# Kernel optimization log

Measured on AMD Instinct MI355X. Metric: run time of the kernel, lower is better.

Reference implementation:

```python
import jax, jax.numpy as jnp
import numpy as np

SEQ = 4096
BLOCK = 64            # sparse_block_size
BLOCKS = SEQ // BLOCK # 64 block rows/cols
NUM_ORACLES = 32
ORACLE = SEQ // NUM_ORACLES      # 128
LOCAL_BLOCKS = ORACLE // BLOCK   # 2 (sliding-window width in blocks)
PATTERN_ID = 0


def _build_block_mask(pattern_id=PATTERN_ID):
    # Mirrors DKernelPredefinedSparseAttention.__init__ create_mask((i,))
    q_pos = np.arange(BLOCKS)[:, None]
    k_pos = np.arange(BLOCKS)[None, :]
    causal = q_pos >= k_pos
    sliding = (q_pos - k_pos) < LOCAL_BLOCKS
    vert = np.zeros(BLOCKS, dtype=bool)
    real_col = int(pattern_id * ORACLE + 0.5)
    cs = real_col // BLOCK
    ce = (real_col + ORACLE) // BLOCK
    vert[cs:ce] = True
    vert[0:1] = True  # global block 0 always visible
    return causal & (sliding | vert[None, :])


def setup_inputs() -> dict:
    key = jax.random.key(0)
    kq, kk, kv = jax.random.split(key, 3)
    shape = (1, SEQ, 8, 128)  # bshd, matches module's own smoke test layout
    q = jax.random.normal(kq, shape, dtype=jnp.float32)
    k = jax.random.normal(kk, shape, dtype=jnp.float32)
    v = jax.random.normal(kv, shape, dtype=jnp.float32)
    block_mask = jnp.asarray(_build_block_mask())  # [BLOCKS, BLOCKS] bool
    return {"q": q, "k": k, "v": v, "block_mask": block_mask}


def reference(q, k, v, block_mask):
    # Expand block-level mask to token level: [S, S]
    tok_mask = jnp.repeat(jnp.repeat(block_mask, BLOCK, axis=0), BLOCK, axis=1)
    scale = 1.0 / jnp.sqrt(jnp.asarray(q.shape[-1], q.dtype))
    # bshd x bshd -> bhqk scores
    scores = jnp.einsum("bqhd,bkhd->bhqk", q, k) * scale
    neg = jnp.asarray(-1e30, scores.dtype)
    scores = jnp.where(tok_mask[None, None, :, :], scores, neg)
    probs = jax.nn.softmax(scores, axis=-1)
    out = jnp.einsum("bhqk,bkhd->bqhd", probs, v)
    return out
```

## Files before the change

### kernel.cpp

```cpp
#include <hip/hip_runtime.h>
#include <hip/hip_bf16.h>

typedef __bf16 bf16x8 __attribute__((ext_vector_type(8)));
typedef float floatx4 __attribute__((ext_vector_type(4)));

constexpr int SEQ = 4096;
constexpr int NH  = 8;
constexpr int DH  = 128;
constexpr int BLK = 64;
constexpr int QBLOCKS = SEQ / BLK;
constexpr int RS = NH * DH;
constexpr float SCALE = 0.088388347648318447f;

__device__ __forceinline__ bf16x8 load8f(const float* p) {
    float4 a = *(const float4*)p;
    float4 b = *(const float4*)(p + 4);
    bf16x8 r = { (__bf16)a.x, (__bf16)a.y, (__bf16)a.z, (__bf16)a.w,
                 (__bf16)b.x, (__bf16)b.y, (__bf16)b.z, (__bf16)b.w };
    return r;
}

__device__ __forceinline__ void stage_v(const float* __restrict__ V,
                                        int kb, int h, int n_t, int kh,
                                        __bf16* __restrict__ dst) {
    const float* base = V + (size_t)(kb * BLK + kh * 32) * RS + h * DH + n_t;
    const int nt = n_t >> 4;
    const int lbase = n_t & 15;
#pragma unroll
    for (int g = 0; g < 4; ++g) {
        bf16x8 pk;
#pragma unroll
        for (int j = 0; j < 8; ++j)
            pk[j] = (__bf16)base[(size_t)(g * 8 + j) * RS];
        __bf16* d = dst + ((size_t)((kh * 8 + nt) * 64 + lbase + 16 * g)) * 8;
        *(bf16x8*)d = pk;
    }
}

__global__ __launch_bounds__(256) void sparse_attn_kernel(
    const float* __restrict__ Q,
    const float* __restrict__ K,
    const float* __restrict__ V,
    float* __restrict__ Out)
{
    const int qb   = blockIdx.x;
    const int h    = blockIdx.y;
    const int tid  = threadIdx.x;
    const int wave = tid >> 6;
    const int lane = tid & 63;
    const int quad = lane >> 4;
    const int l16  = lane & 15;

    __shared__ __align__(16) __bf16 v_lds[2][2][8][64][8];
    __shared__ __align__(16) __bf16 p_lds[4][16][BLK + 8];

    const int n_t = tid & 127;
    const int kh  = tid >> 7;

    const int qrow = qb * BLK + wave * 16 + l16;
    const float* qp = Q + (size_t)qrow * RS + h * DH;
    bf16x8 qfrag[4];
#pragma unroll
    for (int s = 0; s < 4; ++s)
        qfrag[s] = load8f(qp + s * 32 + quad * 8);

    floatx4 o_acc[8];
#pragma unroll
    for (int n = 0; n < 8; ++n) o_acc[n] = floatx4{0.f, 0.f, 0.f, 0.f};
    float m_run[4], l_run[4];
#pragma unroll
    for (int r = 0; r < 4; ++r) { m_run[r] = -1e30f; l_run[r] = 0.f; }

    int blist[4];
    int nb = 0;
    {
        int cand[4] = {0, 1, qb - 1, qb};
        for (int i = 0; i < 4; ++i) {
            int b = cand[i];
            if (b < 0 || b > qb) continue;
            bool dup = false;
            for (int j = 0; j < nb; ++j) dup = dup || (blist[j] == b);
            if (!dup) blist[nb++] = b;
        }
    }

    stage_v(V, blist[0], h, n_t, kh, &v_lds[0][0][0][0][0]);

    for (int bi = 0; bi < nb; ++bi) {
        __syncthreads();
        if (bi + 1 < nb)
            stage_v(V, blist[bi + 1], h, n_t, kh,
                    &v_lds[(bi + 1) & 1][0][0][0][0]);

        const int kb  = blist[bi];
        const int buf = bi & 1;

        floatx4 sfrag[4];
#pragma unroll
        for (int n = 0; n < 4; ++n) {
            floatx4 c = floatx4{0.f, 0.f, 0.f, 0.f};
            const float* kp =
                K + (size_t)(kb * BLK + n * 16 + l16) * RS + h * DH;
#pragma unroll
            for (int s = 0; s < 4; ++s) {
                bf16x8 kf = load8f(kp + s * 32 + quad * 8);
                c = __builtin_amdgcn_mfma_f32_16x16x32_bf16(qfrag[s], kf, c, 0, 0, 0);
            }
            sfrag[n] = c;
        }

        float mnew[4];
#pragma unroll
        for (int r = 0; r < 4; ++r) {
            float mx = m_run[r];
#pragma unroll
            for (int n = 0; n < 4; ++n) {
                sfrag[n][r] *= SCALE;
                mx = fmaxf(mx, sfrag[n][r]);
            }
#pragma unroll
            for (int off = 1; off < 16; off <<= 1)
                mx = fmaxf(mx, __shfl_xor(mx, off, 64));
            mnew[r] = mx;
        }
#pragma unroll
        for (int r = 0; r < 4; ++r) {
            float alpha = __expf(m_run[r] - mnew[r]);
            float rs = 0.f;
#pragma unroll
            for (int n = 0; n < 4; ++n) {
                float p = __expf(sfrag[n][r] - mnew[r]);
                sfrag[n][r] = p;
                rs += p;
            }
#pragma unroll
            for (int off = 1; off < 16; off <<= 1)
                rs += __shfl_xor(rs, off, 64);
            l_run[r] = l_run[r] * alpha + rs;
            m_run[r] = mnew[r];
#pragma unroll
            for (int n = 0; n < 8; ++n) o_acc[n][r] *= alpha;
        }

#pragma unroll
        for (int n = 0; n < 4; ++n)
#pragma unroll
            for (int r = 0; r < 4; ++r)
                p_lds[wave][quad * 4 + r][n * 16 + l16] = (__bf16)sfrag[n][r];

#pragma unroll
        for (int s2 = 0; s2 < 2; ++s2) {
            bf16x8 pa = *(const bf16x8*)&p_lds[wave][l16][s2 * 32 + quad * 8];
#pragma unroll
            for (int n = 0; n < 8; ++n) {
                bf16x8 vb = *(const bf16x8*)&v_lds[buf][s2][n][lane][0];
                o_acc[n] = __builtin_amdgcn_mfma_f32_16x16x32_bf16(pa, vb, o_acc[n], 0, 0, 0);
            }
        }
    }

    const int orow_base = qb * BLK + wave * 16 + quad * 4;
#pragma unroll
    for (int r = 0; r < 4; ++r) {
        float inv = 1.f / l_run[r];
        float* op = Out + (size_t)(orow_base + r) * RS + h * DH + l16;
#pragma unroll
        for (int n = 0; n < 8; ++n)
            op[n * 16] = o_acc[n][r] * inv;
    }
}

extern "C" void kernel_launch(void* const* d_in, const int* in_sizes, int n_in,
                              void* d_out, int out_size, void* d_ws, size_t ws_size,
                              hipStream_t stream) {
    const float* Q = (const float*)d_in[0];
    const float* K = (const float*)d_in[1];
    const float* V = (const float*)d_in[2];
    float* Out = (float*)d_out;

    dim3 grid(QBLOCKS, NH);
    dim3 block(256);
    sparse_attn_kernel<<<grid, block, 0, stream>>>(Q, K, V, Out);
}
```

Before: 127.7 us.

## Split key blocks across two wave groups with split-K softmax merge

Doubles the workgroup to 512 threads, with two groups of four waves each handling alternate key blocks for the same query strip. All V blocks are staged into LDS up front instead of double-buffered. Partial softmax states are merged through LDS at the end. The P tile in LDS now uses an XOR swizzle to cut bank conflicts. This raises parallelism and shortens the serial per-block chain, at the cost of extra LDS, a merge step and duplicated Q loads.

```diff
diff --git a/kernel.cpp b/kernel.cpp
--- a/kernel.cpp
+++ b/kernel.cpp
@@ -37,39 +37,24 @@
     }
 }
 
-__global__ __launch_bounds__(256) void sparse_attn_kernel(
+__global__ __launch_bounds__(512, 4) void sparse_attn_kernel(
     const float* __restrict__ Q,
     const float* __restrict__ K,
     const float* __restrict__ V,
     float* __restrict__ Out)
 {
-    const int qb   = blockIdx.x;
-    const int h    = blockIdx.y;
-    const int tid  = threadIdx.x;
-    const int wave = tid >> 6;
-    const int lane = tid & 63;
-    const int quad = lane >> 4;
-    const int l16  = lane & 15;
-
-    __shared__ __align__(16) __bf16 v_lds[2][2][8][64][8];
-    __shared__ __align__(16) __bf16 p_lds[4][16][BLK + 8];
-
-    const int n_t = tid & 127;
-    const int kh  = tid >> 7;
-
-    const int qrow = qb * BLK + wave * 16 + l16;
-    const float* qp = Q + (size_t)qrow * RS + h * DH;
-    bf16x8 qfrag[4];
-#pragma unroll
-    for (int s = 0; s < 4; ++s)
-        qfrag[s] = load8f(qp + s * 32 + quad * 8);
-
-    floatx4 o_acc[8];
-#pragma unroll
-    for (int n = 0; n < 8; ++n) o_acc[n] = floatx4{0.f, 0.f, 0.f, 0.f};
-    float m_run[4], l_run[4];
-#pragma unroll
-    for (int r = 0; r < 4; ++r) { m_run[r] = -1e30f; l_run[r] = 0.f; }
+    const int qb    = blockIdx.x;
+    const int h     = blockIdx.y;
+    const int tid   = threadIdx.x;
+    const int wave  = tid >> 6;
+    const int lane  = tid & 63;
+    const int strip = wave & 3;
+    const int grp   = wave >> 2;
+    const int quad  = lane >> 4;
+    const int l16   = lane & 15;
+
+    __shared__ __align__(16) __bf16 v_lds[4][2][8][64][8];
+    __shared__ __align__(16) __bf16 p_lds[8][16][64];
 
     int blist[4];
     int nb = 0;
@@ -84,89 +69,150 @@
         }
     }
 
-    stage_v(V, blist[0], h, n_t, kh, &v_lds[0][0][0][0][0]);
-
-    for (int bi = 0; bi < nb; ++bi) {
-        __syncthreads();
-        if (bi + 1 < nb)
-            stage_v(V, blist[bi + 1], h, n_t, kh,
-                    &v_lds[(bi + 1) & 1][0][0][0][0]);
-
-        const int kb  = blist[bi];
-        const int buf = bi & 1;
-
-        floatx4 sfrag[4];
-#pragma unroll
-        for (int n = 0; n < 4; ++n) {
-            floatx4 c = floatx4{0.f, 0.f, 0.f, 0.f};
-            const float* kp =
-                K + (size_t)(kb * BLK + n * 16 + l16) * RS + h * DH;
-#pragma unroll
-            for (int s = 0; s < 4; ++s) {
-                bf16x8 kf = load8f(kp + s * 32 + quad * 8);
-                c = __builtin_amdgcn_mfma_f32_16x16x32_bf16(qfrag[s], kf, c, 0, 0, 0);
-            }
-            sfrag[n] = c;
-        }
-
-        float mnew[4];
+    {
+        const int t256 = tid & 255;
+        const int n_t  = t256 & 127;
+        const int kh   = t256 >> 7;
+        const int half = tid >> 8;
+        if (half < nb)
+            stage_v(V, blist[half], h, n_t, kh, &v_lds[half][0][0][0][0]);
+        if (half + 2 < nb)
+            stage_v(V, blist[half + 2], h, n_t, kh, &v_lds[half + 2][0][0][0][0]);
+    }
+
+    const int qrow = qb * BLK + strip * 16 + l16;
+    const float* qp = Q + (size_t)qrow * RS + h * DH;
+    bf16x8 qfrag[4];
+#pragma unroll
+    for (int s = 0; s < 4; ++s)
+        qfrag[s] = load8f(qp + s * 32 + quad * 8);
+
+    floatx4 o_acc[8];
+#pragma unroll
+    for (int n = 0; n < 8; ++n) o_acc[n] = floatx4{0.f, 0.f, 0.f, 0.f};
+    float m_run[4], l_run[4];
+#pragma unroll
+    for (int r = 0; r < 4; ++r) { m_run[r] = -1e30f; l_run[r] = 0.f; }
+
+    __syncthreads();
+
+#pragma unroll
+    for (int it = 0; it < 2; ++it) {
+        const int bi = grp + 2 * it;
+        if (bi < nb) {
+            const int kb = blist[bi];
+
+            floatx4 sfrag[4];
+#pragma unroll
+            for (int n = 0; n < 4; ++n) {
+                floatx4 c = floatx4{0.f, 0.f, 0.f, 0.f};
+                const float* kp =
+                    K + (size_t)(kb * BLK + n * 16 + l16) * RS + h * DH;
+#pragma unroll
+                for (int s = 0; s < 4; ++s) {
+                    bf16x8 kf = load8f(kp + s * 32 + quad * 8);
+                    c = __builtin_amdgcn_mfma_f32_16x16x32_bf16(qfrag[s], kf, c, 0, 0, 0);
+                }
+                sfrag[n] = c;
+            }
+
+            float mnew[4];
+#pragma unroll
+            for (int r = 0; r < 4; ++r) {
+                float mx = m_run[r];
+#pragma unroll
+                for (int n = 0; n < 4; ++n) {
+                    sfrag[n][r] *= SCALE;
+                    mx = fmaxf(mx, sfrag[n][r]);
+                }
+#pragma unroll
+                for (int off = 1; off < 16; off <<= 1)
+                    mx = fmaxf(mx, __shfl_xor(mx, off, 64));
+                mnew[r] = mx;
+            }
+#pragma unroll
+            for (int r = 0; r < 4; ++r) {
+                float alpha = __expf(m_run[r] - mnew[r]);
+                float rs = 0.f;
+#pragma unroll
+                for (int n = 0; n < 4; ++n) {
+                    float p = __expf(sfrag[n][r] - mnew[r]);
+                    sfrag[n][r] = p;
+                    rs += p;
+                }
+#pragma unroll
+                for (int off = 1; off < 16; off <<= 1)
+                    rs += __shfl_xor(rs, off, 64);
+                l_run[r] = l_run[r] * alpha + rs;
+                m_run[r] = mnew[r];
+#pragma unroll
+                for (int n = 0; n < 8; ++n) o_acc[n][r] *= alpha;
+            }
+
+#pragma unroll
+            for (int n = 0; n < 4; ++n)
+#pragma unroll
+                for (int r = 0; r < 4; ++r) {
+                    const int prow = quad * 4 + r;
+                    const int col  = n * 16 + l16;
+                    const int idx  = (((col >> 3) ^ (prow & 7)) << 3) | (col & 7);
+                    p_lds[wave][prow][idx] = (__bf16)sfrag[n][r];
+                }
+
+#pragma unroll
+            for (int s2 = 0; s2 < 2; ++s2) {
+                bf16x8 pa = *(const bf16x8*)
+                    &p_lds[wave][l16][(((s2 * 4 + quad) ^ (l16 & 7)) << 3)];
+#pragma unroll
+                for (int n = 0; n < 8; ++n) {
+                    bf16x8 vb = *(const bf16x8*)&v_lds[bi][s2][n][lane][0];
+                    o_acc[n] = __builtin_amdgcn_mfma_f32_16x16x32_bf16(pa, vb, o_acc[n], 0, 0, 0);
+                }
+            }
+        }
+    }
+
+    __syncthreads();
+
+    float* mrg = (float*)&v_lds[0][0][0][0][0];
+    constexpr int OSTRIDE = 132;
+    constexpr int OSZ     = 16 * OSTRIDE;
+    constexpr int MBASE   = 4 * OSZ;
+    constexpr int LBASE   = MBASE + 64;
+
+    if (grp == 1) {
 #pragma unroll
         for (int r = 0; r < 4; ++r) {
-            float mx = m_run[r];
-#pragma unroll
-            for (int n = 0; n < 4; ++n) {
-                sfrag[n][r] *= SCALE;
-                mx = fmaxf(mx, sfrag[n][r]);
-            }
-#pragma unroll
-            for (int off = 1; off < 16; off <<= 1)
-                mx = fmaxf(mx, __shfl_xor(mx, off, 64));
-            mnew[r] = mx;
-        }
+            if (l16 == 0) {
+                mrg[MBASE + strip * 16 + quad * 4 + r] = m_run[r];
+                mrg[LBASE + strip * 16 + quad * 4 + r] = l_run[r];
+            }
+#pragma unroll
+            for (int n = 0; n < 8; ++n)
+                mrg[strip * OSZ + (quad * 4 + r) * OSTRIDE + n * 16 + l16] =
+                    o_acc[n][r];
+        }
+    }
+    __syncthreads();
+
+    if (grp == 0) {
+        const int orow_base = qb * BLK + strip * 16 + quad * 4;
 #pragma unroll
         for (int r = 0; r < 4; ++r) {
-            float alpha = __expf(m_run[r] - mnew[r]);
-            float rs = 0.f;
-#pragma unroll
-            for (int n = 0; n < 4; ++n) {
-                float p = __expf(sfrag[n][r] - mnew[r]);
-                sfrag[n][r] = p;
-                rs += p;
-            }
-#pragma unroll
-            for (int off = 1; off < 16; off <<= 1)
-                rs += __shfl_xor(rs, off, 64);
-            l_run[r] = l_run[r] * alpha + rs;
-            m_run[r] = mnew[r];
-#pragma unroll
-            for (int n = 0; n < 8; ++n) o_acc[n][r] *= alpha;
-        }
-
-#pragma unroll
-        for (int n = 0; n < 4; ++n)
-#pragma unroll
-            for (int r = 0; r < 4; ++r)
-                p_lds[wave][quad * 4 + r][n * 16 + l16] = (__bf16)sfrag[n][r];
-
-#pragma unroll
-        for (int s2 = 0; s2 < 2; ++s2) {
-            bf16x8 pa = *(const bf16x8*)&p_lds[wave][l16][s2 * 32 + quad * 8];
+            const float m1 = mrg[MBASE + strip * 16 + quad * 4 + r];
+            const float l1 = mrg[LBASE + strip * 16 + quad * 4 + r];
+            const float M  = fmaxf(m_run[r], m1);
+            const float a0 = __expf(m_run[r] - M);
+            const float a1 = __expf(m1 - M);
+            const float inv = 1.f / (a0 * l_run[r] + a1 * l1);
+            float* op = Out + (size_t)(orow_base + r) * RS + h * DH + l16;
 #pragma unroll
             for (int n = 0; n < 8; ++n) {
-                bf16x8 vb = *(const bf16x8*)&v_lds[buf][s2][n][lane][0];
-                o_acc[n] = __builtin_amdgcn_mfma_f32_16x16x32_bf16(pa, vb, o_acc[n], 0, 0, 0);
-            }
-        }
-    }
-
-    const int orow_base = qb * BLK + wave * 16 + quad * 4;
-#pragma unroll
-    for (int r = 0; r < 4; ++r) {
-        float inv = 1.f / l_run[r];
-        float* op = Out + (size_t)(orow_base + r) * RS + h * DH + l16;
-#pragma unroll
-        for (int n = 0; n < 8; ++n)
-            op[n * 16] = o_acc[n][r] * inv;
+                const float o1 =
+                    mrg[strip * OSZ + (quad * 4 + r) * OSTRIDE + n * 16 + l16];
+                op[n * 16] = (a0 * o_acc[n][r] + a1 * o1) * inv;
+            }
+        }
     }
 }
 
@@ -179,6 +225,6 @@
     float* Out = (float*)d_out;
 
     dim3 grid(QBLOCKS, NH);
-    dim3 block(256);
+    dim3 block(512);
     sparse_attn_kernel<<<grid, block, 0, stream>>>(Q, K, V, Out);
 }
```

Measured after the change: 127.3 us. Within noise of the previous version (-0.3%).
